# Kernel optimization log

Hardware: AMD Instinct MI355X
Metric: run time of the kernel (lower is better)

## Reference

```python
import jax, jax.numpy as jnp
import numpy as np

WINDOW = 9
PAD = (WINDOW - 1) // 2


def setup_inputs() -> dict:
    key = jax.random.key(0)
    k1, k2 = jax.random.split(key)
    B, C, L, H = 32, 512, 4096, 8
    x = jax.random.normal(k1, (B, C, L), dtype=jnp.float32)
    W = jax.random.normal(k2, (H, C, WINDOW), dtype=jnp.float32) * (1.0 / np.sqrt(C * WINDOW))
    b = jnp.zeros((H,), dtype=jnp.float32)
    return {"x": x, "W": W, "b": b}


def reference(x, W, b):
    # conv1d: x [B,C,L], W [H,C,w] -> logits [B,H,L] (same padding, stride 1)
    logits = jax.lax.conv_general_dilated(
        x, W,
        window_strides=(1,),
        padding=[(PAD, PAD)],
        dimension_numbers=("NCH", "OIH", "NCH"),
    ) + b[None, :, None]
    # softmax over sequence length
    focus = jax.nn.softmax(logits, axis=-1)  # [B,H,L]
    # per-head weighted sum pooling over L: [B,C,H]
    pooled = jnp.einsum("bhl,bcl->bch", focus, x)
    # reduce='max' over heads -> [B,C]
    return jnp.max(pooled, axis=-1)
```

## Files before the change

kernel.cpp:

```cpp
#include <hip/hip_runtime.h>

#define B_LEN 32
#define C_LEN 512
#define L_LEN 4096
#define H_LEN 8
#define WIN 9

typedef __attribute__((ext_vector_type(8))) short short8v;
typedef __attribute__((ext_vector_type(4))) short short4v;
typedef __attribute__((ext_vector_type(4))) float float4v;

__device__ __forceinline__ short f2bf(float f) {
  unsigned u = __float_as_uint(f);
  unsigned r = (u + 0x7fffu + ((u >> 16) & 1u)) >> 16;
  return (short)r;
}

__device__ __forceinline__ int xoff(int row, int colbyte) {
  return row * 128 + (colbyte ^ (((row >> 1) & 7) << 4));
}

__global__ __launch_bounds__(256) void repack_w_bf16(
    const float* __restrict__ W, short* __restrict__ Wt)
{
  const int i = blockIdx.x * 256 + threadIdx.x;
  if (i >= WIN * 16 * C_LEN) return;
  const int c = i & 511;
  const int h = (i >> 9) & 15;
  const int w = i / (16 * C_LEN);
  const float v = (h < H_LEN) ? W[((size_t)h * C_LEN + c) * WIN + w] : 0.f;
  Wt[i] = f2bf(v);
}

__global__ __launch_bounds__(256) void conv_mfma(
    const float* __restrict__ x, const short* __restrict__ Wt,
    float* __restrict__ part)
{
  __shared__ short xt[2][264 * 64];
  const int t = threadIdx.x;
  const int lane = t & 63;
  const int wid = t >> 6;
  const int j15 = lane & 15;
  const int g = lane >> 4;
  const int g16 = g * 16;
  const int b = blockIdx.y;
  const int l0b = blockIdx.x * 256;
  const float* xb = x + (size_t)b * C_LEN * L_LEN;
  const int wl0 = wid * 64;

  auto STAGE = [&](int buf, int cc2) {
    char* bb = (char*)&xt[buf][0];
    const int lq = t & 63;
    const int cg = t >> 6;
#pragma unroll
    for (int p = 0; p < 4; ++p) {
      const int cl = p * 16 + cg * 4;
      const float* src = xb + (size_t)(cc2 * 64 + cl) * L_LEN + (l0b + 4 * lq);
      const float4 v0 = *reinterpret_cast<const float4*>(src);
      const float4 v1 = *reinterpret_cast<const float4*>(src + L_LEN);
      const float4 v2 = *reinterpret_cast<const float4*>(src + 2 * L_LEN);
      const float4 v3 = *reinterpret_cast<const float4*>(src + 3 * L_LEN);
      const int colb = cl * 2;
      const short4v r0 = { f2bf(v0.x), f2bf(v1.x), f2bf(v2.x), f2bf(v3.x) };
      const short4v r1 = { f2bf(v0.y), f2bf(v1.y), f2bf(v2.y), f2bf(v3.y) };
      const short4v r2 = { f2bf(v0.z), f2bf(v1.z), f2bf(v2.z), f2bf(v3.z) };
      const short4v r3 = { f2bf(v0.w), f2bf(v1.w), f2bf(v2.w), f2bf(v3.w) };
      *(short4v*)(bb + xoff(4 * lq + 4, colb)) = r0;
      *(short4v*)(bb + xoff(4 * lq + 5, colb)) = r1;
      *(short4v*)(bb + xoff(4 * lq + 6, colb)) = r2;
      *(short4v*)(bb + xoff(4 * lq + 7, colb)) = r3;
    }
    if (t < 32) {
      const int c4 = t & 15;
      const int side = t >> 4;
      const int cl = c4 * 4;
      const int gl = side ? (l0b + 256) : (l0b - 4);
      const bool ok = side ? (l0b + 256 < L_LEN) : (l0b > 0);
      float4 v0 = make_float4(0.f, 0.f, 0.f, 0.f), v1 = v0, v2 = v0, v3 = v0;
      if (ok) {
        const float* src = xb + (size_t)(cc2 * 64 + cl) * L_LEN + gl;
        v0 = *reinterpret_cast<const float4*>(src);
        v1 = *reinterpret_cast<const float4*>(src + L_LEN);
        v2 = *reinterpret_cast<const float4*>(src + 2 * L_LEN);
        v3 = *reinterpret_cast<const float4*>(src + 3 * L_LEN);
      }
      const int colb = cl * 2;
      const int r = side ? 260 : 0;
      const short4v r0 = { f2bf(v0.x), f2bf(v1.x), f2bf(v2.x), f2bf(v3.x) };
      const short4v r1 = { f2bf(v0.y), f2bf(v1.y), f2bf(v2.y), f2bf(v3.y) };
      const short4v r2 = { f2bf(v0.z), f2bf(v1.z), f2bf(v2.z), f2bf(v3.z) };
      const short4v r3 = { f2bf(v0.w), f2bf(v1.w), f2bf(v2.w), f2bf(v3.w) };
      *(short4v*)(bb + xoff(r + 0, colb)) = r0;
      *(short4v*)(bb + xoff(r + 1, colb)) = r1;
      *(short4v*)(bb + xoff(r + 2, colb)) = r2;
      *(short4v*)(bb + xoff(r + 3, colb)) = r3;
    }
  };

  float4v acc0 = {0.f, 0.f, 0.f, 0.f};
  float4v acc1 = acc0, acc2 = acc0, acc3 = acc0;
  const int wlane = j15 * C_LEN + 8 * g;

  STAGE(0, 0);
  __syncthreads();

  for (int cc = 0; cc < 8; ++cc) {
    if (cc < 7) STAGE((cc + 1) & 1, cc + 1);
    const char* base = (const char*)&xt[cc & 1][0];
    const short* Wc = Wt + cc * 64 + wlane;
    short8v wf0 = *(const short8v*)(Wc);
    short8v wf1 = *(const short8v*)(Wc + 32);
#pragma unroll
    for (int w = 0; w < WIN; ++w) {
      short8v wn0 = wf0, wn1 = wf1;
      if (w + 1 < WIN) {
        wn0 = *(const short8v*)(Wc + (w + 1) * (16 * C_LEN));
        wn1 = *(const short8v*)(Wc + (w + 1) * (16 * C_LEN) + 32);
      }
      const int rbase = wl0 + j15 + w;
#define MSTEP(SUB, ACC)                                                        \
      {                                                                        \
        short8v xfa = *(const short8v*)(base + xoff(rbase + SUB * 16, g16));   \
        ACC = __builtin_amdgcn_mfma_f32_16x16x32_bf16(wf0, xfa, ACC, 0, 0, 0); \
        short8v xfb = *(const short8v*)(base + xoff(rbase + SUB * 16, 64 + g16)); \
        ACC = __builtin_amdgcn_mfma_f32_16x16x32_bf16(wf1, xfb, ACC, 0, 0, 0); \
      }
      MSTEP(0, acc0) MSTEP(1, acc1) MSTEP(2, acc2) MSTEP(3, acc3)
#undef MSTEP
      wf0 = wn0; wf1 = wn1;
    }
    __syncthreads();
  }

  if (lane < 32) {
    float* d = part + ((size_t)b * H_LEN + 4 * g) * L_LEN + (l0b + wl0 + j15);
#pragma unroll
    for (int r = 0; r < 4; ++r) {
      d[(size_t)r * L_LEN +  0] = acc0[r];
      d[(size_t)r * L_LEN + 16] = acc1[r];
      d[(size_t)r * L_LEN + 32] = acc2[r];
      d[(size_t)r * L_LEN + 48] = acc3[r];
    }
  }
}

__global__ __launch_bounds__(256) void softmax_rows(
    const float* __restrict__ part, float* __restrict__ focus)
{
  __shared__ float red[256];
  const int r = blockIdx.x;
  const int t = threadIdx.x;
  float v[16];
#pragma unroll
  for (int k = 0; k < 4; ++k) {
    const int i4 = (t + 256 * k) * 4;
    float4 a = *reinterpret_cast<const float4*>(&part[(size_t)r * L_LEN + i4]);
    v[4 * k + 0] = a.x; v[4 * k + 1] = a.y; v[4 * k + 2] = a.z; v[4 * k + 3] = a.w;
  }
  float m = v[0];
#pragma unroll
  for (int k = 1; k < 16; ++k) m = fmaxf(m, v[k]);
  red[t] = m;
  __syncthreads();
  for (int s = 128; s > 0; s >>= 1) {
    if (t < s) red[t] = fmaxf(red[t], red[t + s]);
    __syncthreads();
  }
  m = red[0];
  __syncthreads();
  float sum = 0.f;
#pragma unroll
  for (int k = 0; k < 16; ++k) { v[k] = __expf(v[k] - m); sum += v[k]; }
  red[t] = sum;
  __syncthreads();
  for (int s = 128; s > 0; s >>= 1) {
    if (t < s) red[t] += red[t + s];
    __syncthreads();
  }
  const float inv = 1.f / red[0];
#pragma unroll
  for (int k = 0; k < 4; ++k) {
    const int i4 = (t + 256 * k) * 4;
    float4 a;
    a.x = v[4 * k + 0] * inv; a.y = v[4 * k + 1] * inv;
    a.z = v[4 * k + 2] * inv; a.w = v[4 * k + 3] * inv;
    *reinterpret_cast<float4*>(&focus[(size_t)r * L_LEN + i4]) = a;
  }
}

#define K3_ST 68
#define K3_NS 4

__global__ __launch_bounds__(256) void pool_partial(
    const float* __restrict__ x, const float* __restrict__ focus,
    float* __restrict__ pool2)
{
  __shared__ float xs[64 * K3_ST];
  const int t = threadIdx.x;
  const int cl = t & 63;
  const int p = t >> 6;
  const int pu = __builtin_amdgcn_readfirstlane(p);
  const int b = blockIdx.y;
  const int c0 = blockIdx.x * 64;
  const int lbeg = blockIdx.z * (L_LEN / K3_NS);
  const float* f0 = focus + ((size_t)b * H_LEN + pu) * L_LEN;
  const float* f1 = f0 + 4 * (size_t)L_LEN;
  const float* xb = x + (size_t)b * C_LEN * L_LEN;
  const int srow = t >> 4;
  const int scol = (t & 15) * 4;
  float acc0 = 0.f, acc1 = 0.f;

  for (int l0 = lbeg; l0 < lbeg + L_LEN / K3_NS; l0 += 64) {
    __syncthreads();
#pragma unroll
    for (int pass = 0; pass < 4; ++pass) {
      const int c = srow + pass * 16;
      float4 v = *reinterpret_cast<const float4*>(&xb[(size_t)(c0 + c) * L_LEN + l0 + scol]);
      *reinterpret_cast<float4*>(&xs[c * K3_ST + scol]) = v;
    }
    __syncthreads();
#pragma unroll
    for (int l4 = 0; l4 < 16; ++l4) {
      const float4 xv = *reinterpret_cast<const float4*>(&xs[cl * K3_ST + 4 * l4]);
      const int li = l0 + 4 * l4;
      acc0 = fmaf(xv.x, f0[li + 0], acc0);
      acc0 = fmaf(xv.y, f0[li + 1], acc0);
      acc0 = fmaf(xv.z, f0[li + 2], acc0);
      acc0 = fmaf(xv.w, f0[li + 3], acc0);
      acc1 = fmaf(xv.x, f1[li + 0], acc1);
      acc1 = fmaf(xv.y, f1[li + 1], acc1);
      acc1 = fmaf(xv.z, f1[li + 2], acc1);
      acc1 = fmaf(xv.w, f1[li + 3], acc1);
    }
  }
  float* dst = pool2 + (((size_t)blockIdx.z * B_LEN + b) * C_LEN + c0 + cl) * H_LEN;
  dst[p] = acc0;
  dst[p + 4] = acc1;
}

__global__ __launch_bounds__(256) void pool_reduce(
    const float* __restrict__ pool2, float* __restrict__ out)
{
  const int i = blockIdx.x * 256 + threadIdx.x;
  float s[H_LEN];
#pragma unroll
  for (int h = 0; h < H_LEN; ++h) s[h] = 0.f;
  for (int ls = 0; ls < K3_NS; ++ls) {
    const float* src = pool2 + ((size_t)ls * B_LEN * C_LEN + i) * H_LEN;
    float4 a = *reinterpret_cast<const float4*>(src);
    float4 b4 = *reinterpret_cast<const float4*>(src + 4);
    s[0] += a.x; s[1] += a.y; s[2] += a.z; s[3] += a.w;
    s[4] += b4.x; s[5] += b4.y; s[6] += b4.z; s[7] += b4.w;
  }
  float m = s[0];
#pragma unroll
  for (int h = 1; h < H_LEN; ++h) m = fmaxf(m, s[h]);
  out[i] = m;
}

extern "C" void kernel_launch(void* const* d_in, const int* in_sizes, int n_in,
                              void* d_out, int out_size, void* d_ws, size_t ws_size,
                              hipStream_t stream)
{
  const float* x = (const float*)d_in[0];
  const float* W = (const float*)d_in[1];
  float* out = (float*)d_out;
  float* ws = (float*)d_ws;

  const size_t PART = (size_t)B_LEN * H_LEN * L_LEN;
  const size_t POOL2N = (size_t)K3_NS * B_LEN * C_LEN * H_LEN;

  float* part = ws;
  float* focus = ws + PART;
  float* pool2 = focus + PART;
  short* Wt = (short*)(pool2 + POOL2N);

  hipLaunchKernelGGL(repack_w_bf16, dim3((WIN * 16 * C_LEN + 255) / 256), dim3(256), 0,
                     stream, W, Wt);
  hipLaunchKernelGGL(conv_mfma, dim3(L_LEN / 256, B_LEN), dim3(256), 0,
                     stream, x, Wt, part);
  hipLaunchKernelGGL(softmax_rows, dim3(B_LEN * H_LEN), dim3(256), 0,
                     stream, part, focus);
  hipLaunchKernelGGL(pool_partial, dim3(C_LEN / 64, B_LEN, K3_NS), dim3(256), 0,
                     stream, x, focus, pool2);
  hipLaunchKernelGGL(pool_reduce, dim3((B_LEN * C_LEN) / 256), dim3(256), 0,
                     stream, pool2, out);
}
```

Baseline: 139.9 us.

## Give each wave a private LDS slice and drop block-level barriers in conv

The conv MFMA kernel now has each wave stage its own 64-column tile plus halo into a private double-buffered LDS slice, in 32-channel chunks with a new swizzle. It software-pipelines global loads in registers against MFMA compute, which removes every __syncthreads. LDS per block shrinks, and launch bounds now request 3 blocks per CU to raise occupancy. In exchange, each wave reloads its own halo columns, and the halo stores are scalar 2-byte LDS writes.

```diff
diff --git a/kernel.cpp b/kernel.cpp
--- a/kernel.cpp
+++ b/kernel.cpp
@@ -7,17 +7,12 @@
 #define WIN 9
 
 typedef __attribute__((ext_vector_type(8))) short short8v;
-typedef __attribute__((ext_vector_type(4))) short short4v;
 typedef __attribute__((ext_vector_type(4))) float float4v;
 
 __device__ __forceinline__ short f2bf(float f) {
   unsigned u = __float_as_uint(f);
   unsigned r = (u + 0x7fffu + ((u >> 16) & 1u)) >> 16;
   return (short)r;
-}
-
-__device__ __forceinline__ int xoff(int row, int colbyte) {
-  return row * 128 + (colbyte ^ (((row >> 1) & 7) << 4));
 }
 
 __global__ __launch_bounds__(256) void repack_w_bf16(
@@ -32,11 +27,13 @@
   Wt[i] = f2bf(v);
 }
 
-__global__ __launch_bounds__(256) void conv_mfma(
+#define SLICE 5760
+
+__global__ __launch_bounds__(256, 3) void conv_mfma(
     const float* __restrict__ x, const short* __restrict__ Wt,
     float* __restrict__ part)
 {
-  __shared__ short xt[2][264 * 64];
+  __shared__ short xt[4 * 2 * (SLICE / 2)];
   const int t = threadIdx.x;
   const int lane = t & 63;
   const int wid = t >> 6;
@@ -45,91 +42,94 @@
   const int g16 = g * 16;
   const int b = blockIdx.y;
   const int l0b = blockIdx.x * 256;
+  const int wl0 = wid * 64;
+  const int s = l0b + wl0 - 4;
   const float* xb = x + (size_t)b * C_LEN * L_LEN;
-  const int wl0 = wid * 64;
-
-  auto STAGE = [&](int buf, int cc2) {
-    char* bb = (char*)&xt[buf][0];
-    const int lq = t & 63;
-    const int cg = t >> 6;
-#pragma unroll
-    for (int p = 0; p < 4; ++p) {
-      const int cl = p * 16 + cg * 4;
-      const float* src = xb + (size_t)(cc2 * 64 + cl) * L_LEN + (l0b + 4 * lq);
-      const float4 v0 = *reinterpret_cast<const float4*>(src);
-      const float4 v1 = *reinterpret_cast<const float4*>(src + L_LEN);
-      const float4 v2 = *reinterpret_cast<const float4*>(src + 2 * L_LEN);
-      const float4 v3 = *reinterpret_cast<const float4*>(src + 3 * L_LEN);
-      const int colb = cl * 2;
-      const short4v r0 = { f2bf(v0.x), f2bf(v1.x), f2bf(v2.x), f2bf(v3.x) };
-      const short4v r1 = { f2bf(v0.y), f2bf(v1.y), f2bf(v2.y), f2bf(v3.y) };
-      const short4v r2 = { f2bf(v0.z), f2bf(v1.z), f2bf(v2.z), f2bf(v3.z) };
-      const short4v r3 = { f2bf(v0.w), f2bf(v1.w), f2bf(v2.w), f2bf(v3.w) };
-      *(short4v*)(bb + xoff(4 * lq + 4, colb)) = r0;
-      *(short4v*)(bb + xoff(4 * lq + 5, colb)) = r1;
-      *(short4v*)(bb + xoff(4 * lq + 6, colb)) = r2;
-      *(short4v*)(bb + xoff(4 * lq + 7, colb)) = r3;
-    }
-    if (t < 32) {
-      const int c4 = t & 15;
-      const int side = t >> 4;
-      const int cl = c4 * 4;
-      const int gl = side ? (l0b + 256) : (l0b - 4);
-      const bool ok = side ? (l0b + 256 < L_LEN) : (l0b > 0);
-      float4 v0 = make_float4(0.f, 0.f, 0.f, 0.f), v1 = v0, v2 = v0, v3 = v0;
-      if (ok) {
-        const float* src = xb + (size_t)(cc2 * 64 + cl) * L_LEN + gl;
-        v0 = *reinterpret_cast<const float4*>(src);
-        v1 = *reinterpret_cast<const float4*>(src + L_LEN);
-        v2 = *reinterpret_cast<const float4*>(src + 2 * L_LEN);
-        v3 = *reinterpret_cast<const float4*>(src + 3 * L_LEN);
-      }
-      const int colb = cl * 2;
-      const int r = side ? 260 : 0;
-      const short4v r0 = { f2bf(v0.x), f2bf(v1.x), f2bf(v2.x), f2bf(v3.x) };
-      const short4v r1 = { f2bf(v0.y), f2bf(v1.y), f2bf(v2.y), f2bf(v3.y) };
-      const short4v r2 = { f2bf(v0.z), f2bf(v1.z), f2bf(v2.z), f2bf(v3.z) };
-      const short4v r3 = { f2bf(v0.w), f2bf(v1.w), f2bf(v2.w), f2bf(v3.w) };
-      *(short4v*)(bb + xoff(r + 0, colb)) = r0;
-      *(short4v*)(bb + xoff(r + 1, colb)) = r1;
-      *(short4v*)(bb + xoff(r + 2, colb)) = r2;
-      *(short4v*)(bb + xoff(r + 3, colb)) = r3;
-    }
-  };
+
+  char* bufA = (char*)&xt[0] + (size_t)wid * 2 * SLICE;
+  char* bufB = bufA + SLICE;
+
+  const int q = lane & 15;
+  const int chigh = lane >> 4;
+  const int bl = s + 4 + 4 * q;
+  const int hside = lane >> 5;
+  const int hc = lane & 31;
+  const int hl = s + (hside ? 68 : 0);
+  const bool hok = (hl >= 0) && (hl + 3 < L_LEN);
+  const int hlc = hok ? hl : (hside ? (L_LEN - 4) : 0);
+  const int hr = hside ? 68 : 0;
+  const int hkey = hside ? 16 : 0;
+
+  float4 L0, L1, L2, L3, L4, L5, L6, L7, LH;
+  const float4 z4 = make_float4(0.f, 0.f, 0.f, 0.f);
+
+#define LOADK(K)                                                               \
+  {                                                                            \
+    const float* bsrc = xb + (size_t)((K) * 32 + chigh * 8) * L_LEN + bl;      \
+    L0 = *(const float4*)(bsrc);                                               \
+    L1 = *(const float4*)(bsrc + 1 * (size_t)L_LEN);                           \
+    L2 = *(const float4*)(bsrc + 2 * (size_t)L_LEN);                           \
+    L3 = *(const float4*)(bsrc + 3 * (size_t)L_LEN);                           \
+    L4 = *(const float4*)(bsrc + 4 * (size_t)L_LEN);                           \
+    L5 = *(const float4*)(bsrc + 5 * (size_t)L_LEN);                           \
+    L6 = *(const float4*)(bsrc + 6 * (size_t)L_LEN);                           \
+    L7 = *(const float4*)(bsrc + 7 * (size_t)L_LEN);                           \
+    LH = *(const float4*)(xb + (size_t)((K) * 32 + hc) * L_LEN + hlc);         \
+    if (!hok) LH = z4;                                                         \
+  }
+
+#define WROW(BB, E, CMP)                                                       \
+  {                                                                            \
+    const int r = 4 + 4 * q + (E);                                             \
+    short8v v = { f2bf(L0.CMP), f2bf(L1.CMP), f2bf(L2.CMP), f2bf(L3.CMP),      \
+                  f2bf(L4.CMP), f2bf(L5.CMP), f2bf(L6.CMP), f2bf(L7.CMP) };    \
+    *(short8v*)((BB) + r * 80 + ((chigh * 16) ^ (((r >> 2) & 3) << 4))) = v;   \
+  }
+
+#define WRITEB(BB)                                                             \
+  {                                                                            \
+    WROW(BB, 0, x) WROW(BB, 1, y) WROW(BB, 2, z) WROW(BB, 3, w)                \
+    *(short*)((BB) + (hr + 0) * 80 + ((hc * 2) ^ hkey)) = f2bf(LH.x);          \
+    *(short*)((BB) + (hr + 1) * 80 + ((hc * 2) ^ hkey)) = f2bf(LH.y);          \
+    *(short*)((BB) + (hr + 2) * 80 + ((hc * 2) ^ hkey)) = f2bf(LH.z);          \
+    *(short*)((BB) + (hr + 3) * 80 + ((hc * 2) ^ hkey)) = f2bf(LH.w);          \
+  }
+
+#define MSTEP(BB, ROFF, ACC)                                                   \
+  {                                                                            \
+    const int r = rw + (ROFF);                                                 \
+    short8v xf = *(const short8v*)((BB) + r * 80 + (g16 ^ (((r >> 2) & 3) << 4))); \
+    ACC = __builtin_amdgcn_mfma_f32_16x16x32_bf16(wf, xf, ACC, 0, 0, 0);       \
+  }
+
+#define COMPUTE(BB, K)                                                         \
+  {                                                                            \
+    const short* Wb = Wt + (K) * 32 + j15 * 512 + 8 * g;                       \
+    short8v wf = *(const short8v*)(Wb);                                        \
+    _Pragma("unroll") for (int w = 0; w < 9; ++w) {                            \
+      short8v wn = wf;                                                         \
+      if (w < 8) wn = *(const short8v*)(Wb + (w + 1) * (16 * C_LEN));          \
+      const int rw = j15 + w;                                                  \
+      MSTEP(BB, 0, acc0) MSTEP(BB, 16, acc1)                                   \
+      MSTEP(BB, 32, acc2) MSTEP(BB, 48, acc3)                                  \
+      wf = wn;                                                                 \
+    }                                                                          \
+  }
 
   float4v acc0 = {0.f, 0.f, 0.f, 0.f};
   float4v acc1 = acc0, acc2 = acc0, acc3 = acc0;
-  const int wlane = j15 * C_LEN + 8 * g;
-
-  STAGE(0, 0);
-  __syncthreads();
-
-  for (int cc = 0; cc < 8; ++cc) {
-    if (cc < 7) STAGE((cc + 1) & 1, cc + 1);
-    const char* base = (const char*)&xt[cc & 1][0];
-    const short* Wc = Wt + cc * 64 + wlane;
-    short8v wf0 = *(const short8v*)(Wc);
-    short8v wf1 = *(const short8v*)(Wc + 32);
-#pragma unroll
-    for (int w = 0; w < WIN; ++w) {
-      short8v wn0 = wf0, wn1 = wf1;
-      if (w + 1 < WIN) {
-        wn0 = *(const short8v*)(Wc + (w + 1) * (16 * C_LEN));
-        wn1 = *(const short8v*)(Wc + (w + 1) * (16 * C_LEN) + 32);
-      }
-      const int rbase = wl0 + j15 + w;
-#define MSTEP(SUB, ACC)                                                        \
-      {                                                                        \
-        short8v xfa = *(const short8v*)(base + xoff(rbase + SUB * 16, g16));   \
-        ACC = __builtin_amdgcn_mfma_f32_16x16x32_bf16(wf0, xfa, ACC, 0, 0, 0); \
-        short8v xfb = *(const short8v*)(base + xoff(rbase + SUB * 16, 64 + g16)); \
-        ACC = __builtin_amdgcn_mfma_f32_16x16x32_bf16(wf1, xfb, ACC, 0, 0, 0); \
-      }
-      MSTEP(0, acc0) MSTEP(1, acc1) MSTEP(2, acc2) MSTEP(3, acc3)
-#undef MSTEP
-      wf0 = wn0; wf1 = wn1;
-    }
-    __syncthreads();
+
+  LOADK(0)
+  WRITEB(bufA)
+
+  for (int k8 = 0; k8 < 8; ++k8) {
+    const int kk = 2 * k8;
+    LOADK(kk + 1)
+    COMPUTE(bufA, kk)
+    WRITEB(bufB)
+    if (k8 < 7) { LOADK(kk + 2) }
+    COMPUTE(bufB, kk + 1)
+    if (k8 < 7) { WRITEB(bufA) }
   }
 
   if (lane < 32) {
@@ -142,6 +142,11 @@
       d[(size_t)r * L_LEN + 48] = acc3[r];
     }
   }
+#undef LOADK
+#undef WROW
+#undef WRITEB
+#undef MSTEP
+#undef COMPUTE
 }
 
 __global__ __launch_bounds__(256) void softmax_rows(
```

Result: no change. 141.5 us (+1.2%).
